# Performance work log

Hardware: AMD Instinct MI355X
Metric: run time of the kernel (lower is better)

Reference implementation:

```python
import jax, jax.numpy as jnp
import numpy as np

D, W, H = 128, 128, 128          # volume obj_shape (d, w, h)
RES_SCALE = 1.4
RES_D = int(D * RES_SCALE)       # 179 detector rows
RES_H = int(H * RES_SCALE)       # 179 detector cols
N_PROJ = 10


def setup_inputs() -> dict:
    key = jax.random.key(0)
    k1, k2 = jax.random.split(key, 2)
    # learnable reconstruction volume, initialized to ones (torch.ones_like)
    I_rec = jnp.ones((1, 1, D, W, H), dtype=jnp.float32)
    # emitter positions, scaled to volume size; y-component kept away from the
    # source plane y=0 so that ray directions are well-conditioned
    poses = jax.random.uniform(k1, (50, 3), dtype=jnp.float32)
    poses = poses * jnp.array([D, W, H], jnp.float32) + jnp.array([-64.0, 256.0, -64.0], jnp.float32)
    idx = jax.random.randint(k2, (N_PROJ,), 0, 50, dtype=jnp.int32)
    return {"I_rec": I_rec, "poses": poses, "idx": idx}


def _trilinear_3d(vol, coords):
    """torch F.grid_sample 3D, bilinear, align_corners=False, zero padding.
    vol: [D, Hd, Wd]; coords: [..., 3] in (x, y, z) normalized to [-1, 1],
    where x indexes the last (Wd) axis, y the middle, z the first."""
    Dv, Hv, Wv = vol.shape
    x, y, z = coords[..., 0], coords[..., 1], coords[..., 2]
    ix = ((x + 1.0) * Wv - 1.0) * 0.5
    iy = ((y + 1.0) * Hv - 1.0) * 0.5
    iz = ((z + 1.0) * Dv - 1.0) * 0.5
    x0f, y0f, z0f = jnp.floor(ix), jnp.floor(iy), jnp.floor(iz)
    tx, ty, tz = ix - x0f, iy - y0f, iz - z0f
    x0 = x0f.astype(jnp.int32); y0 = y0f.astype(jnp.int32); z0 = z0f.astype(jnp.int32)
    x1, y1, z1 = x0 + 1, y0 + 1, z0 + 1

    def gather(zc, yc, xc):
        valid = (zc >= 0) & (zc < Dv) & (yc >= 0) & (yc < Hv) & (xc >= 0) & (xc < Wv)
        v = vol[jnp.clip(zc, 0, Dv - 1), jnp.clip(yc, 0, Hv - 1), jnp.clip(xc, 0, Wv - 1)]
        return jnp.where(valid, v, 0.0)

    out = (
        gather(z0, y0, x0) * (1 - tz) * (1 - ty) * (1 - tx)
        + gather(z0, y0, x1) * (1 - tz) * (1 - ty) * tx
        + gather(z0, y1, x0) * (1 - tz) * ty * (1 - tx)
        + gather(z0, y1, x1) * (1 - tz) * ty * tx
        + gather(z1, y0, x0) * tz * (1 - ty) * (1 - tx)
        + gather(z1, y0, x1) * tz * (1 - ty) * tx
        + gather(z1, y1, x0) * tz * ty * (1 - tx)
        + gather(z1, y1, x1) * tz * ty * tx
    )
    return out


def _project_one(vol, emi):
    """vol: [D, W, H]; emi: [3] emitter position. Returns [RES_D, RES_H]."""
    lin_x = jnp.linspace(-RES_D / 2.0, RES_D / 2.0 - 1.0, RES_D, dtype=jnp.float32)
    lin_y = jnp.linspace(-RES_H / 2.0, RES_H / 2.0 - 1.0, RES_H, dtype=jnp.float32)
    gx, gy = jnp.meshgrid(lin_x, lin_y, indexing="ij")            # [Gx, Gy]
    rays = jnp.stack([gx, jnp.zeros_like(gx), gy], axis=-1) - emi  # [Gx, Gy, 3]
    rays = rays / jnp.linalg.norm(rays, axis=-1, keepdims=True)
    dx = jnp.abs(1.0 / rays[..., 1])                               # [Gx, Gy]
    # (P0 - I0) . N  with N = (0,1,0): source-plane y samples minus emitter y
    p0y = jnp.linspace(0.0, W - 1.0, W, dtype=jnp.float32)         # [K=W]
    T = (1.0 / rays[..., 1])[..., None] * (p0y - emi[1])           # [Gx, Gy, K]
    grid = rays[..., None, :] * T[..., None] + emi                 # [Gx, Gy, K, 3]
    g0 = grid[..., 0] / D * 2.0
    g1 = grid[..., 1] / W * 2.0 - 1.0
    g2 = grid[..., 2] / H * 2.0
    coords = jnp.stack([g2, g1, g0], axis=-1)  # torch.flip(grid, [3]) -> (x,y,z)
    samp = _trilinear_3d(vol, coords)          # [Gx, Gy, K]
    return jnp.sum(samp, axis=-1) * dx


def reference(I_rec, poses, idx):
    sel = poses[idx]  # [10, 3]
    vol = I_rec[0, 0]
    projections = jax.vmap(lambda e: _project_one(vol, e))(sel)  # [10, Gx, Gy]
    return projections[None], idx
```

## Files before the change

### kernel.cpp

```cpp
#include <hip/hip_runtime.h>
#include <hip/hip_bf16.h>
#include <stdint.h>


#define DVOL   128
#define RES    179
#define NPROJ  10
#define OUT_PROJ (NPROJ * RES * RES)
#define BATCH  8

#define IL_A   132
#define IL_C   130
#define IL_SLAB (IL_C * IL_A)
#define IL_TOT  (DVOL * IL_SLAB)

__device__ __forceinline__ float psval(const float* __restrict__ vol, int p, int r, int ai) {
    const int c = r - 1, a = ai - 1;
    if (c < 0 || c >= 128 || a < 0 || a >= 128) return 0.0f;
    const float* src = vol + (c << 14) + (p << 7) + a;
    float v = src[0];
    if (p >= 1) v += src[-128];
    return v;
}

__device__ __forceinline__ uint32_t bfbits(float v) {
    __hip_bfloat16 h = __float2bfloat16(v);
    return (uint32_t)*(unsigned short*)&h;
}

__global__ __launch_bounds__(256) void pad_kernel(const float* __restrict__ vol,
                                                  uint32_t* __restrict__ il) {
    const int t = blockIdx.x * 256 + threadIdx.x;
    if (t >= IL_TOT) return;
    const int p  = t / IL_SLAB;
    const int r  = t - p * IL_SLAB;
    const int ci = r / IL_A;
    const int ai = r - ci * IL_A;
    const float lo = psval(vol, p, ci,     ai);
    const float hi = psval(vol, p, ci + 1, ai);
    il[t] = (bfbits(hi) << 16) | bfbits(lo);
}

__device__ __forceinline__ void axis_interval(float base, float slope, float lo, float hi,
                                              float& t0, float& t1) {
    if (fabsf(slope) < 1e-9f) {
        const bool in = (base >= lo && base <= hi);
        t0 = in ? -1e30f : 1e30f;
        t1 = in ?  1e30f : -1e30f;
    } else {
        const float inv = 1.0f / slope;
        const float a = (lo - base) * inv;
        const float b = (hi - base) * inv;
        t0 = fminf(a, b);
        t1 = fmaxf(a, b);
    }
}

__device__ __forceinline__ int wave_imin(int v) {
    #pragma unroll
    for (int o = 32; o; o >>= 1) v = min(v, __shfl_xor(v, o, 64));
    return v;
}
__device__ __forceinline__ int wave_imax(int v) {
    #pragma unroll
    for (int o = 32; o; o >>= 1) v = max(v, __shfl_xor(v, o, 64));
    return v;
}

__device__ __forceinline__ float asf(uint32_t u) { return __uint_as_float(u); }

__global__ __launch_bounds__(128) void proj_fast(
    const uint32_t* __restrict__ il,
    const float* __restrict__ poses,
    const int* __restrict__ idx,
    float* __restrict__ out)
{
    const int lane = threadIdx.x & 63;
    const int wid  = threadIdx.x >> 6;
    int gj = blockIdx.x * 64 + lane;
    int gi = blockIdx.y * 2 + wid;
    const int j = blockIdx.z;

    if (blockIdx.x == 0 && blockIdx.y == 0 && j == 0 && threadIdx.x < NPROJ)
        out[OUT_PROJ + threadIdx.x] = (float)idx[threadIdx.x];

    const bool store_ok = (gi < RES) && (gj < RES);
    gi = min(gi, RES - 1);
    gj = min(gj, RES - 1);

    const int pid = idx[j];
    const float ex = poses[pid * 3 + 0];
    const float ey = poses[pid * 3 + 1];
    const float ez = poses[pid * 3 + 2];

    const float pdx = (float)gi - 89.5f;
    const float pdz = (float)gj - 89.5f;

    const float inv_ey = 1.0f / ey;
    const float sx = (ex - pdx) * inv_ey;
    const float sz = (ez - pdz) * inv_ey;
    const float ddx = pdx - ex, ddz = pdz - ez;
    const float dxw = sqrtf(ddx * ddx + ey * ey + ddz * ddz) * fabsf(inv_ey);
    const float cb = pdx + 63.5f;
    const float ab = pdz + 63.5f;

    float gc0, gc1, ga0, ga1;
    axis_interval(cb, sx, -1.0f, 128.0f, gc0, gc1);
    axis_interval(ab, sz, -1.0f, 128.0f, ga0, ga1);
    const float q_lo = fmaxf(fmaxf(gc0, ga0), 0.0f);
    const float q_hi = fminf(fminf(gc1, ga1), 127.0f);
    int q0, q1;
    if (q_lo <= q_hi + 0.5f) {
        q0 = max(0, (int)ceilf(q_lo) - 1);
        q1 = min(DVOL, (int)floorf(q_hi) + 2);
    } else { q0 = DVOL; q1 = 0; }
    int Q0 = wave_imin(q0);
    int Q1 = wave_imax(q1);
    Q0 = __builtin_amdgcn_readfirstlane(Q0);
    Q1 = __builtin_amdgcn_readfirstlane(Q1);

    float acc = 0.0f;
    int p = Q0;
    float cf = fmaf((float)Q0, sx, cb);
    float af = fmaf((float)Q0, sz, ab);
    const uint32_t* slab = il + Q0 * IL_SLAB;

    for (; p + (BATCH - 1) < Q1; p += BATCH) {
        float tc[BATCH], ta[BATCH];
        uint2 w[BATCH];
        #pragma unroll
        for (int k = 0; k < BATCH; ++k) {
            const float cfc = fminf(fmaxf(fmaf((float)k, sx, cf), -1.0f), 128.0f);
            const float afc = fminf(fmaxf(fmaf((float)k, sz, af), -1.0f), 128.0f);
            const float c0f = floorf(cfc);
            const float a0f = floorf(afc);
            tc[k] = cfc - c0f;
            ta[k] = afc - a0f;
            const int c0 = __builtin_amdgcn_readfirstlane((int)c0f);
            const int a0 = (int)a0f;
            const uint32_t* wr = slab + k * IL_SLAB + (c0 + 1) * IL_A + 1;
            w[k] = *(const uint2*)(wr + a0);
        }
        #pragma unroll
        for (int k = 0; k < BATCH; ++k) {
            const float f00 = asf(w[k].x << 16);
            const float f10 = asf(w[k].x & 0xffff0000u);
            const float f01 = asf(w[k].y << 16);
            const float f11 = asf(w[k].y & 0xffff0000u);
            const float h0 = fmaf(ta[k], f01 - f00, f00);
            const float h1 = fmaf(ta[k], f11 - f10, f10);
            acc += fmaf(tc[k], h1 - h0, h0);
        }
        cf += (float)BATCH * sx;
        af += (float)BATCH * sz;
        slab += BATCH * IL_SLAB;
    }
    for (; p < Q1; ++p) {
        const float cfc = fminf(fmaxf(cf, -1.0f), 128.0f);
        const float afc = fminf(fmaxf(af, -1.0f), 128.0f);
        const float c0f = floorf(cfc);
        const float a0f = floorf(afc);
        const float tc = cfc - c0f;
        const float ta = afc - a0f;
        const int c0 = __builtin_amdgcn_readfirstlane((int)c0f);
        const int a0 = (int)a0f;
        const uint32_t* wr = slab + (c0 + 1) * IL_A + 1;
        const uint2 w2 = *(const uint2*)(wr + a0);
        const float f00 = asf(w2.x << 16);
        const float f10 = asf(w2.x & 0xffff0000u);
        const float f01 = asf(w2.y << 16);
        const float f11 = asf(w2.y & 0xffff0000u);
        const float h0 = fmaf(ta, f01 - f00, f00);
        const float h1 = fmaf(ta, f11 - f10, f10);
        acc += fmaf(tc, h1 - h0, h0);
        cf += sx; af += sz; slab += IL_SLAB;
    }

    if (store_ok) out[j * (RES * RES) + gi * RES + gj] = acc * (0.5f * dxw);
}

__global__ __launch_bounds__(256) void proj_kernel_fb(
    const float* __restrict__ vol, const float* __restrict__ poses,
    const int* __restrict__ idx, float* __restrict__ out)
{
    const int gj = blockIdx.x * 64 + (threadIdx.x & 63);
    const int gi = blockIdx.y * 4 + (threadIdx.x >> 6);
    const int j  = blockIdx.z;
    if (blockIdx.x == 0 && blockIdx.y == 0 && j == 0 && threadIdx.x < NPROJ)
        out[OUT_PROJ + threadIdx.x] = (float)idx[threadIdx.x];
    if (gi >= RES || gj >= RES) return;
    const int pid = idx[j];
    const float ex = poses[pid*3+0], ey = poses[pid*3+1], ez = poses[pid*3+2];
    const float pdx = (float)gi - 89.5f, pdz = (float)gj - 89.5f;
    const float inv_ey = 1.0f / ey;
    const float sx = (ex - pdx) * inv_ey, sz = (ez - pdz) * inv_ey;
    const float ddx = pdx - ex, ddz = pdz - ez;
    const float dxw = sqrtf(ddx*ddx + ey*ey + ddz*ddz) * fabsf(inv_ey);
    const float cb = pdx + 63.5f, ab = pdz + 63.5f;
    float acc = 0.0f;
    for (int p = 0; p < DVOL; ++p) {
        const float cf = fmaf((float)p, sx, cb);
        const float af = fmaf((float)p, sz, ab);
        if (cf >= -1.0f && cf < 128.0f && af >= -1.0f && af < 128.0f) {
            const float c0f = floorf(cf), a0f = floorf(af);
            const float tc = cf - c0f, ta = af - a0f;
            const int c0 = (int)c0f, a0 = (int)a0f;
            const float wc0 = (c0 >= 0)   ? (1.0f - tc) : 0.0f;
            const float wc1 = (c0 <= 126) ? tc          : 0.0f;
            const float wa0 = (a0 >= 0)   ? (1.0f - ta) : 0.0f;
            const float wa1 = (a0 <= 126) ? ta          : 0.0f;
            const int c0c = c0 < 0 ? 0 : c0;
            const int c1c = c0 >= 127 ? 127 : c0 + 1;
            const int a0c = a0 < 0 ? 0 : a0;
            const int a1c = a0 >= 127 ? 127 : a0 + 1;
            const float w00 = wc0*wa0, w01 = wc0*wa1, w10 = wc1*wa0, w11 = wc1*wa1;
            const int b0 = (c0c << 14) + (p << 7);
            const int b1 = (c1c << 14) + (p << 7);
            float s = w00*vol[b0+a0c] + w01*vol[b0+a1c] + w10*vol[b1+a0c] + w11*vol[b1+a1c];
            if (p >= 1)
                s += w00*vol[b0+a0c-128] + w01*vol[b0+a1c-128]
                   + w10*vol[b1+a0c-128] + w11*vol[b1+a1c-128];
            acc += 0.5f * s;
        }
    }
    out[j * (RES * RES) + gi * RES + gj] = acc * dxw;
}

extern "C" void kernel_launch(void* const* d_in, const int* in_sizes, int n_in,
                              void* d_out, int out_size, void* d_ws, size_t ws_size,
                              hipStream_t stream) {
    const float* vol   = (const float*)d_in[0];
    const float* poses = (const float*)d_in[1];
    const int*   idx   = (const int*)d_in[2];
    float* out = (float*)d_out;

    if (ws_size >= (size_t)IL_TOT * sizeof(uint32_t)) {
        uint32_t* ilbuf = (uint32_t*)d_ws;
        pad_kernel<<<IL_TOT / 256, 256, 0, stream>>>(vol, ilbuf);
        dim3 grid(3 , 90 , NPROJ);
        proj_fast<<<grid, 128, 0, stream>>>(ilbuf, poses, idx, out);
    } else {
        dim3 grid(3, 45, NPROJ);
        proj_kernel_fb<<<grid, 256, 0, stream>>>(vol, poses, idx, out);
    }
}
```

Baseline: 101.4 us.

## Split each ray's depth range across two waves and double-buffer sample loads

Each block now handles one detector row, and its two waves each take half of the ray's depth range. The partial sums are combined through shared memory after a barrier. The batched loop is also restructured to double-buffer: the next 8-sample batch's gathers are issued before the current batch is interpolated, which hides load latency. The grid doubles in the row dimension, and the change adds a __syncthreads, shared memory, and higher register pressure from holding two batches.

```diff
diff --git a/kernel.cpp b/kernel.cpp
--- a/kernel.cpp
+++ b/kernel.cpp
@@ -7,7 +7,6 @@
 #define RES    179
 #define NPROJ  10
 #define OUT_PROJ (NPROJ * RES * RES)
-#define BATCH  8
 
 #define IL_A   132
 #define IL_C   130
@@ -69,23 +68,61 @@
 
 __device__ __forceinline__ float asf(uint32_t u) { return __uint_as_float(u); }
 
+struct B8 { float tc[8], ta[8]; uint2 w[8]; };
+
+__device__ __forceinline__ void load_b8(B8& b, const uint32_t* __restrict__ il, int p,
+                                        float cb, float ab, float sx, float sz) {
+    const uint32_t* slab = il + p * IL_SLAB;
+    const float cf = fmaf((float)p, sx, cb);
+    const float af = fmaf((float)p, sz, ab);
+    #pragma unroll
+    for (int k = 0; k < 8; ++k) {
+        const float cfc = fminf(fmaxf(fmaf((float)k, sx, cf), -1.0f), 128.0f);
+        const float afc = fminf(fmaxf(fmaf((float)k, sz, af), -1.0f), 128.0f);
+        const float c0f = floorf(cfc);
+        const float a0f = floorf(afc);
+        b.tc[k] = cfc - c0f;
+        b.ta[k] = afc - a0f;
+        const int c0 = __builtin_amdgcn_readfirstlane((int)c0f);
+        const int a0 = (int)a0f;
+        const uint32_t* wr = slab + k * IL_SLAB + (c0 + 1) * IL_A + 1;
+        b.w[k] = *(const uint2*)(wr + a0);
+    }
+}
+
+__device__ __forceinline__ float comp_b8(const B8& b) {
+    float s = 0.0f;
+    #pragma unroll
+    for (int k = 0; k < 8; ++k) {
+        const float f00 = asf(b.w[k].x << 16);
+        const float f10 = asf(b.w[k].x & 0xffff0000u);
+        const float f01 = asf(b.w[k].y << 16);
+        const float f11 = asf(b.w[k].y & 0xffff0000u);
+        const float h0 = fmaf(b.ta[k], f01 - f00, f00);
+        const float h1 = fmaf(b.ta[k], f11 - f10, f10);
+        s += fmaf(b.tc[k], h1 - h0, h0);
+    }
+    return s;
+}
+
 __global__ __launch_bounds__(128) void proj_fast(
     const uint32_t* __restrict__ il,
     const float* __restrict__ poses,
     const int* __restrict__ idx,
     float* __restrict__ out)
 {
+    __shared__ float part[64];
+
     const int lane = threadIdx.x & 63;
     const int wid  = threadIdx.x >> 6;
     int gj = blockIdx.x * 64 + lane;
-    int gi = blockIdx.y * 2 + wid;
-    const int j = blockIdx.z;
+    const int gi = blockIdx.y;
+    const int j  = blockIdx.z;
 
     if (blockIdx.x == 0 && blockIdx.y == 0 && j == 0 && threadIdx.x < NPROJ)
         out[OUT_PROJ + threadIdx.x] = (float)idx[threadIdx.x];
 
-    const bool store_ok = (gi < RES) && (gj < RES);
-    gi = min(gi, RES - 1);
+    const bool store_ok = (gj < RES);
     gj = min(gj, RES - 1);
 
     const int pid = idx[j];
@@ -119,52 +156,44 @@
     Q0 = __builtin_amdgcn_readfirstlane(Q0);
     Q1 = __builtin_amdgcn_readfirstlane(Q1);
 
+    const int len = max(0, Q1 - Q0);
+    const int mid = Q0 + (len >> 1);
+    const int r0 = wid ? mid : Q0;
+    const int r1 = wid ? Q1 : mid;
+
     float acc = 0.0f;
-    int p = Q0;
-    float cf = fmaf((float)Q0, sx, cb);
-    float af = fmaf((float)Q0, sz, ab);
-    const uint32_t* slab = il + Q0 * IL_SLAB;
-
-    for (; p + (BATCH - 1) < Q1; p += BATCH) {
-        float tc[BATCH], ta[BATCH];
-        uint2 w[BATCH];
-        #pragma unroll
-        for (int k = 0; k < BATCH; ++k) {
-            const float cfc = fminf(fmaxf(fmaf((float)k, sx, cf), -1.0f), 128.0f);
-            const float afc = fminf(fmaxf(fmaf((float)k, sz, af), -1.0f), 128.0f);
-            const float c0f = floorf(cfc);
-            const float a0f = floorf(afc);
-            tc[k] = cfc - c0f;
-            ta[k] = afc - a0f;
-            const int c0 = __builtin_amdgcn_readfirstlane((int)c0f);
-            const int a0 = (int)a0f;
-            const uint32_t* wr = slab + k * IL_SLAB + (c0 + 1) * IL_A + 1;
-            w[k] = *(const uint2*)(wr + a0);
+    int p = r0;
+    const int nfull = (r1 - r0) >> 3;
+
+    if (nfull > 0) {
+        B8 A, Bb;
+        load_b8(A, il, p, cb, ab, sx, sz);
+        int remaining = nfull;
+        while (remaining >= 2) {
+            load_b8(Bb, il, p + 8, cb, ab, sx, sz);
+            acc += comp_b8(A);
+            p += 8; --remaining;
+            if (remaining >= 2) {
+                load_b8(A, il, p + 8, cb, ab, sx, sz);
+                acc += comp_b8(Bb);
+                p += 8; --remaining;
+            } else {
+                acc += comp_b8(Bb);
+                p += 8; --remaining;
+            }
         }
-        #pragma unroll
-        for (int k = 0; k < BATCH; ++k) {
-            const float f00 = asf(w[k].x << 16);
-            const float f10 = asf(w[k].x & 0xffff0000u);
-            const float f01 = asf(w[k].y << 16);
-            const float f11 = asf(w[k].y & 0xffff0000u);
-            const float h0 = fmaf(ta[k], f01 - f00, f00);
-            const float h1 = fmaf(ta[k], f11 - f10, f10);
-            acc += fmaf(tc[k], h1 - h0, h0);
-        }
-        cf += (float)BATCH * sx;
-        af += (float)BATCH * sz;
-        slab += BATCH * IL_SLAB;
-    }
-    for (; p < Q1; ++p) {
-        const float cfc = fminf(fmaxf(cf, -1.0f), 128.0f);
-        const float afc = fminf(fmaxf(af, -1.0f), 128.0f);
+        if (remaining == 1) { acc += comp_b8(A); p += 8; }
+    }
+    for (; p < r1; ++p) {
+        const float cfc = fminf(fmaxf(fmaf((float)p, sx, cb), -1.0f), 128.0f);
+        const float afc = fminf(fmaxf(fmaf((float)p, sz, ab), -1.0f), 128.0f);
         const float c0f = floorf(cfc);
         const float a0f = floorf(afc);
         const float tc = cfc - c0f;
         const float ta = afc - a0f;
         const int c0 = __builtin_amdgcn_readfirstlane((int)c0f);
         const int a0 = (int)a0f;
-        const uint32_t* wr = slab + (c0 + 1) * IL_A + 1;
+        const uint32_t* wr = il + p * IL_SLAB + (c0 + 1) * IL_A + 1;
         const uint2 w2 = *(const uint2*)(wr + a0);
         const float f00 = asf(w2.x << 16);
         const float f10 = asf(w2.x & 0xffff0000u);
@@ -173,10 +202,12 @@
         const float h0 = fmaf(ta, f01 - f00, f00);
         const float h1 = fmaf(ta, f11 - f10, f10);
         acc += fmaf(tc, h1 - h0, h0);
-        cf += sx; af += sz; slab += IL_SLAB;
-    }
-
-    if (store_ok) out[j * (RES * RES) + gi * RES + gj] = acc * (0.5f * dxw);
+    }
+
+    if (wid == 1) part[lane] = acc;
+    __syncthreads();
+    if (wid == 0 && store_ok)
+        out[j * (RES * RES) + gi * RES + gj] = (acc + part[lane]) * (0.5f * dxw);
 }
 
 __global__ __launch_bounds__(256) void proj_kernel_fb(
@@ -237,7 +268,7 @@
     if (ws_size >= (size_t)IL_TOT * sizeof(uint32_t)) {
         uint32_t* ilbuf = (uint32_t*)d_ws;
         pad_kernel<<<IL_TOT / 256, 256, 0, stream>>>(vol, ilbuf);
-        dim3 grid(3 , 90 , NPROJ);
+        dim3 grid(3 , RES, NPROJ);
         proj_fast<<<grid, 128, 0, stream>>>(ilbuf, poses, idx, out);
     } else {
         dim3 grid(3, 45, NPROJ);
```

Measured after the change: 105.8 us. 4.4% more time.

## Convert projection kernel to persistent wave loop and index pad kernel by 2D grid

Applied to the files above, without the earlier changes.

The projection kernel now launches a fixed grid of 2048 blocks, and each wave strides over (x-tile, row, projection) work items instead of getting one per block. The old grid also launched a padding row when RES is odd, which is now gone. The pad kernel uses a 2D grid over (row, slab), which removes the per-thread integer divisions. Together these aim to cut launch and tail overhead and index arithmetic, at the cost of a modulo/divide per item and possibly worse load balance between waves with different ray lengths.

```diff
diff --git a/kernel.cpp b/kernel.cpp
--- a/kernel.cpp
+++ b/kernel.cpp
@@ -13,6 +13,10 @@
 #define IL_C   130
 #define IL_SLAB (IL_C * IL_A)
 #define IL_TOT  (DVOL * IL_SLAB)
+
+#define ITEMS  (3 * RES * NPROJ)
+#define PBLK   2048
+#define PWAVES (PBLK * 2)
 
 __device__ __forceinline__ float psval(const float* __restrict__ vol, int p, int r, int ai) {
     const int c = r - 1, a = ai - 1;
@@ -28,17 +32,23 @@
     return (uint32_t)*(unsigned short*)&h;
 }
 
-__global__ __launch_bounds__(256) void pad_kernel(const float* __restrict__ vol,
+__global__ __launch_bounds__(128) void pad_kernel(const float* __restrict__ vol,
                                                   uint32_t* __restrict__ il) {
-    const int t = blockIdx.x * 256 + threadIdx.x;
-    if (t >= IL_TOT) return;
-    const int p  = t / IL_SLAB;
-    const int r  = t - p * IL_SLAB;
-    const int ci = r / IL_A;
-    const int ai = r - ci * IL_A;
-    const float lo = psval(vol, p, ci,     ai);
-    const float hi = psval(vol, p, ci + 1, ai);
-    il[t] = (bfbits(hi) << 16) | bfbits(lo);
+    const int ci = blockIdx.x;
+    const int p  = blockIdx.y;
+    const int t  = threadIdx.x;
+    const int base = p * IL_SLAB + ci * IL_A;
+    {
+        const float lo = psval(vol, p, ci,     t);
+        const float hi = psval(vol, p, ci + 1, t);
+        il[base + t] = (bfbits(hi) << 16) | bfbits(lo);
+    }
+    if (t < IL_A - 128) {
+        const int ai = 128 + t;
+        const float lo = psval(vol, p, ci,     ai);
+        const float hi = psval(vol, p, ci + 1, ai);
+        il[base + ai] = (bfbits(hi) << 16) | bfbits(lo);
+    }
 }
 
 __device__ __forceinline__ void axis_interval(float base, float slope, float lo, float hi,
@@ -69,114 +79,118 @@
 
 __device__ __forceinline__ float asf(uint32_t u) { return __uint_as_float(u); }
 
-__global__ __launch_bounds__(128) void proj_fast(
+__global__ __launch_bounds__(128) void proj_persist(
     const uint32_t* __restrict__ il,
     const float* __restrict__ poses,
     const int* __restrict__ idx,
     float* __restrict__ out)
 {
-    const int lane = threadIdx.x & 63;
-    const int wid  = threadIdx.x >> 6;
-    int gj = blockIdx.x * 64 + lane;
-    int gi = blockIdx.y * 2 + wid;
-    const int j = blockIdx.z;
-
-    if (blockIdx.x == 0 && blockIdx.y == 0 && j == 0 && threadIdx.x < NPROJ)
+    const int lane  = threadIdx.x & 63;
+    const int wslot = (blockIdx.x << 1) | (threadIdx.x >> 6);
+
+    if (blockIdx.x == 0 && threadIdx.x < NPROJ)
         out[OUT_PROJ + threadIdx.x] = (float)idx[threadIdx.x];
 
-    const bool store_ok = (gi < RES) && (gj < RES);
-    gi = min(gi, RES - 1);
-    gj = min(gj, RES - 1);
-
-    const int pid = idx[j];
-    const float ex = poses[pid * 3 + 0];
-    const float ey = poses[pid * 3 + 1];
-    const float ez = poses[pid * 3 + 2];
-
-    const float pdx = (float)gi - 89.5f;
-    const float pdz = (float)gj - 89.5f;
-
-    const float inv_ey = 1.0f / ey;
-    const float sx = (ex - pdx) * inv_ey;
-    const float sz = (ez - pdz) * inv_ey;
-    const float ddx = pdx - ex, ddz = pdz - ez;
-    const float dxw = sqrtf(ddx * ddx + ey * ey + ddz * ddz) * fabsf(inv_ey);
-    const float cb = pdx + 63.5f;
-    const float ab = pdz + 63.5f;
-
-    float gc0, gc1, ga0, ga1;
-    axis_interval(cb, sx, -1.0f, 128.0f, gc0, gc1);
-    axis_interval(ab, sz, -1.0f, 128.0f, ga0, ga1);
-    const float q_lo = fmaxf(fmaxf(gc0, ga0), 0.0f);
-    const float q_hi = fminf(fminf(gc1, ga1), 127.0f);
-    int q0, q1;
-    if (q_lo <= q_hi + 0.5f) {
-        q0 = max(0, (int)ceilf(q_lo) - 1);
-        q1 = min(DVOL, (int)floorf(q_hi) + 2);
-    } else { q0 = DVOL; q1 = 0; }
-    int Q0 = wave_imin(q0);
-    int Q1 = wave_imax(q1);
-    Q0 = __builtin_amdgcn_readfirstlane(Q0);
-    Q1 = __builtin_amdgcn_readfirstlane(Q1);
-
-    float acc = 0.0f;
-    int p = Q0;
-    float cf = fmaf((float)Q0, sx, cb);
-    float af = fmaf((float)Q0, sz, ab);
-    const uint32_t* slab = il + Q0 * IL_SLAB;
-
-    for (; p + (BATCH - 1) < Q1; p += BATCH) {
-        float tc[BATCH], ta[BATCH];
-        uint2 w[BATCH];
-        #pragma unroll
-        for (int k = 0; k < BATCH; ++k) {
-            const float cfc = fminf(fmaxf(fmaf((float)k, sx, cf), -1.0f), 128.0f);
-            const float afc = fminf(fmaxf(fmaf((float)k, sz, af), -1.0f), 128.0f);
+    for (int item = wslot; item < ITEMS; item += PWAVES) {
+        const int xtile = item % 3;
+        const int rest  = item / 3;
+        const int gi    = rest % RES;
+        const int j     = rest / RES;
+
+        int gj = xtile * 64 + lane;
+        const bool store_ok = (gj < RES);
+        gj = min(gj, RES - 1);
+
+        const int pid = idx[j];
+        const float ex = poses[pid * 3 + 0];
+        const float ey = poses[pid * 3 + 1];
+        const float ez = poses[pid * 3 + 2];
+
+        const float pdx = (float)gi - 89.5f;
+        const float pdz = (float)gj - 89.5f;
+
+        const float inv_ey = 1.0f / ey;
+        const float sx = (ex - pdx) * inv_ey;
+        const float sz = (ez - pdz) * inv_ey;
+        const float ddx = pdx - ex, ddz = pdz - ez;
+        const float dxw = sqrtf(ddx * ddx + ey * ey + ddz * ddz) * fabsf(inv_ey);
+        const float cb = pdx + 63.5f;
+        const float ab = pdz + 63.5f;
+
+        float gc0, gc1, ga0, ga1;
+        axis_interval(cb, sx, -1.0f, 128.0f, gc0, gc1);
+        axis_interval(ab, sz, -1.0f, 128.0f, ga0, ga1);
+        const float q_lo = fmaxf(fmaxf(gc0, ga0), 0.0f);
+        const float q_hi = fminf(fminf(gc1, ga1), 127.0f);
+        int q0, q1;
+        if (q_lo <= q_hi + 0.5f) {
+            q0 = max(0, (int)ceilf(q_lo) - 1);
+            q1 = min(DVOL, (int)floorf(q_hi) + 2);
+        } else { q0 = DVOL; q1 = 0; }
+        int Q0 = wave_imin(q0);
+        int Q1 = wave_imax(q1);
+        Q0 = __builtin_amdgcn_readfirstlane(Q0);
+        Q1 = __builtin_amdgcn_readfirstlane(Q1);
+
+        float acc = 0.0f;
+        int p = Q0;
+        float cf = fmaf((float)Q0, sx, cb);
+        float af = fmaf((float)Q0, sz, ab);
+        const uint32_t* slab = il + Q0 * IL_SLAB;
+
+        for (; p + (BATCH - 1) < Q1; p += BATCH) {
+            float tc[BATCH], ta[BATCH];
+            uint2 w[BATCH];
+            #pragma unroll
+            for (int k = 0; k < BATCH; ++k) {
+                const float cfc = fminf(fmaxf(fmaf((float)k, sx, cf), -1.0f), 128.0f);
+                const float afc = fminf(fmaxf(fmaf((float)k, sz, af), -1.0f), 128.0f);
+                const float c0f = floorf(cfc);
+                const float a0f = floorf(afc);
+                tc[k] = cfc - c0f;
+                ta[k] = afc - a0f;
+                const int c0 = __builtin_amdgcn_readfirstlane((int)c0f);
+                const int a0 = (int)a0f;
+                const uint32_t* wr = slab + k * IL_SLAB + (c0 + 1) * IL_A + 1;
+                w[k] = *(const uint2*)(wr + a0);
+            }
+            #pragma unroll
+            for (int k = 0; k < BATCH; ++k) {
+                const float f00 = asf(w[k].x << 16);
+                const float f10 = asf(w[k].x & 0xffff0000u);
+                const float f01 = asf(w[k].y << 16);
+                const float f11 = asf(w[k].y & 0xffff0000u);
+                const float h0 = fmaf(ta[k], f01 - f00, f00);
+                const float h1 = fmaf(ta[k], f11 - f10, f10);
+                acc += fmaf(tc[k], h1 - h0, h0);
+            }
+            cf += (float)BATCH * sx;
+            af += (float)BATCH * sz;
+            slab += BATCH * IL_SLAB;
+        }
+        for (; p < Q1; ++p) {
+            const float cfc = fminf(fmaxf(cf, -1.0f), 128.0f);
+            const float afc = fminf(fmaxf(af, -1.0f), 128.0f);
             const float c0f = floorf(cfc);
             const float a0f = floorf(afc);
-            tc[k] = cfc - c0f;
-            ta[k] = afc - a0f;
+            const float tc = cfc - c0f;
+            const float ta = afc - a0f;
             const int c0 = __builtin_amdgcn_readfirstlane((int)c0f);
             const int a0 = (int)a0f;
-            const uint32_t* wr = slab + k * IL_SLAB + (c0 + 1) * IL_A + 1;
-            w[k] = *(const uint2*)(wr + a0);
+            const uint32_t* wr = slab + (c0 + 1) * IL_A + 1;
+            const uint2 w2 = *(const uint2*)(wr + a0);
+            const float f00 = asf(w2.x << 16);
+            const float f10 = asf(w2.x & 0xffff0000u);
+            const float f01 = asf(w2.y << 16);
+            const float f11 = asf(w2.y & 0xffff0000u);
+            const float h0 = fmaf(ta, f01 - f00, f00);
+            const float h1 = fmaf(ta, f11 - f10, f10);
+            acc += fmaf(tc, h1 - h0, h0);
+            cf += sx; af += sz; slab += IL_SLAB;
         }
-        #pragma unroll
-        for (int k = 0; k < BATCH; ++k) {
-            const float f00 = asf(w[k].x << 16);
-            const float f10 = asf(w[k].x & 0xffff0000u);
-            const float f01 = asf(w[k].y << 16);
-            const float f11 = asf(w[k].y & 0xffff0000u);
-            const float h0 = fmaf(ta[k], f01 - f00, f00);
-            const float h1 = fmaf(ta[k], f11 - f10, f10);
-            acc += fmaf(tc[k], h1 - h0, h0);
-        }
-        cf += (float)BATCH * sx;
-        af += (float)BATCH * sz;
-        slab += BATCH * IL_SLAB;
-    }
-    for (; p < Q1; ++p) {
-        const float cfc = fminf(fmaxf(cf, -1.0f), 128.0f);
-        const float afc = fminf(fmaxf(af, -1.0f), 128.0f);
-        const float c0f = floorf(cfc);
-        const float a0f = floorf(afc);
-        const float tc = cfc - c0f;
-        const float ta = afc - a0f;
-        const int c0 = __builtin_amdgcn_readfirstlane((int)c0f);
-        const int a0 = (int)a0f;
-        const uint32_t* wr = slab + (c0 + 1) * IL_A + 1;
-        const uint2 w2 = *(const uint2*)(wr + a0);
-        const float f00 = asf(w2.x << 16);
-        const float f10 = asf(w2.x & 0xffff0000u);
-        const float f01 = asf(w2.y << 16);
-        const float f11 = asf(w2.y & 0xffff0000u);
-        const float h0 = fmaf(ta, f01 - f00, f00);
-        const float h1 = fmaf(ta, f11 - f10, f10);
-        acc += fmaf(tc, h1 - h0, h0);
-        cf += sx; af += sz; slab += IL_SLAB;
-    }
-
-    if (store_ok) out[j * (RES * RES) + gi * RES + gj] = acc * (0.5f * dxw);
+
+        if (store_ok) out[j * (RES * RES) + gi * RES + gj] = acc * (0.5f * dxw);
+    }
 }
 
 __global__ __launch_bounds__(256) void proj_kernel_fb(
@@ -236,9 +250,9 @@
 
     if (ws_size >= (size_t)IL_TOT * sizeof(uint32_t)) {
         uint32_t* ilbuf = (uint32_t*)d_ws;
-        pad_kernel<<<IL_TOT / 256, 256, 0, stream>>>(vol, ilbuf);
-        dim3 grid(3 , 90 , NPROJ);
-        proj_fast<<<grid, 128, 0, stream>>>(ilbuf, poses, idx, out);
+        dim3 pgrid(IL_C, DVOL);
+        pad_kernel<<<pgrid, 128, 0, stream>>>(vol, ilbuf);
+        proj_persist<<<PBLK, 128, 0, stream>>>(ilbuf, poses, idx, out);
     } else {
         dim3 grid(3, 45, NPROJ);
         proj_kernel_fb<<<grid, 256, 0, stream>>>(vol, poses, idx, out);
```

Result: slower. 106.9 us (+5.4%).

## Restructure pad kernel to reuse column values and precompute per-wave slab offsets in LDS

Applied to the files above, without the earlier changes.

The pad kernel now gives each thread a column strip and walks down rows, carrying the previous row's bf16 value so each volume element is loaded once instead of twice, and it zeroes the border entries explicitly. The projection kernel precomputes, per wave, the per-slab row fraction and base offset into a shared-memory table, so the main loop reads them instead of recomputing the floor/clamp and readfirstlane each step. This trims ALU work in the hot loop and halves global reads in padding, at the cost of an LDS table, an extra prologue pass, and dropping the scalar readfirstlane hint for the row index.

```diff
diff --git a/kernel.cpp b/kernel.cpp
--- a/kernel.cpp
+++ b/kernel.cpp
@@ -14,31 +14,48 @@
 #define IL_SLAB (IL_C * IL_A)
 #define IL_TOT  (DVOL * IL_SLAB)
 
-__device__ __forceinline__ float psval(const float* __restrict__ vol, int p, int r, int ai) {
-    const int c = r - 1, a = ai - 1;
-    if (c < 0 || c >= 128 || a < 0 || a >= 128) return 0.0f;
-    const float* src = vol + (c << 14) + (p << 7) + a;
-    float v = src[0];
-    if (p >= 1) v += src[-128];
-    return v;
-}
-
 __device__ __forceinline__ uint32_t bfbits(float v) {
     __hip_bfloat16 h = __float2bfloat16(v);
     return (uint32_t)*(unsigned short*)&h;
 }
 
-__global__ __launch_bounds__(256) void pad_kernel(const float* __restrict__ vol,
+__global__ __launch_bounds__(128) void pad_kernel(const float* __restrict__ vol,
                                                   uint32_t* __restrict__ il) {
-    const int t = blockIdx.x * 256 + threadIdx.x;
-    if (t >= IL_TOT) return;
-    const int p  = t / IL_SLAB;
-    const int r  = t - p * IL_SLAB;
-    const int ci = r / IL_A;
-    const int ai = r - ci * IL_A;
-    const float lo = psval(vol, p, ci,     ai);
-    const float hi = psval(vol, p, ci + 1, ai);
-    il[t] = (bfbits(hi) << 16) | bfbits(lo);
+    const int q = blockIdx.x;
+    const int p = blockIdx.y;
+    const int a = threadIdx.x;
+    const int wlo = q * 17;
+    const int whi = min(130, wlo + 17);
+    uint32_t* slab = il + p * IL_SLAB;
+
+    uint32_t prev = 0;
+    {
+        const int c = wlo - 1;
+        if (c >= 0 && c < 128) {
+            const float* src = vol + (c << 14) + (p << 7) + a;
+            float v = src[0];
+            if (p >= 1) v += src[-128];
+            prev = bfbits(v);
+        }
+    }
+    #pragma unroll 2
+    for (int c = wlo; c < whi; ++c) {
+        uint32_t cur = 0;
+        if (c < 128) {
+            const float* src = vol + (c << 14) + (p << 7) + a;
+            float v = src[0];
+            if (p >= 1) v += src[-128];
+            cur = bfbits(v);
+        }
+        slab[c * IL_A + (a + 1)] = (cur << 16) | prev;
+        prev = cur;
+    }
+    for (int b = a; b < (whi - wlo) * 4; b += 128) {
+        const int w  = wlo + (b >> 2);
+        const int bi = b & 3;
+        const int ai = (bi == 0) ? 0 : (128 + bi);
+        slab[w * IL_A + ai] = 0u;
+    }
 }
 
 __device__ __forceinline__ void axis_interval(float base, float slope, float lo, float hi,
@@ -75,6 +92,8 @@
     const int* __restrict__ idx,
     float* __restrict__ out)
 {
+    __shared__ uint2 tab[2][DVOL];
+
     const int lane = threadIdx.x & 63;
     const int wid  = threadIdx.x >> 6;
     int gj = blockIdx.x * 64 + lane;
@@ -119,27 +138,34 @@
     Q0 = __builtin_amdgcn_readfirstlane(Q0);
     Q1 = __builtin_amdgcn_readfirstlane(Q1);
 
+    const int n = Q1 - Q0;
+    for (int e = lane; e < n; e += 64) {
+        const int p = Q0 + e;
+        const float cfc = fminf(fmaxf(fmaf((float)p, sx, cb), -1.0f), 128.0f);
+        const float c0f = floorf(cfc);
+        const int c0 = (int)c0f;
+        uint2 t;
+        t.x = __float_as_uint(cfc - c0f);
+        t.y = (uint32_t)(p * IL_SLAB + (c0 + 1) * IL_A + 1);
+        tab[wid][e] = t;
+    }
+
     float acc = 0.0f;
-    int p = Q0;
-    float cf = fmaf((float)Q0, sx, cb);
+    int pe = 0;
     float af = fmaf((float)Q0, sz, ab);
-    const uint32_t* slab = il + Q0 * IL_SLAB;
-
-    for (; p + (BATCH - 1) < Q1; p += BATCH) {
+
+    for (; pe + (BATCH - 1) < n; pe += BATCH) {
         float tc[BATCH], ta[BATCH];
         uint2 w[BATCH];
         #pragma unroll
         for (int k = 0; k < BATCH; ++k) {
-            const float cfc = fminf(fmaxf(fmaf((float)k, sx, cf), -1.0f), 128.0f);
+            const uint2 t = tab[wid][pe + k];
+            tc[k] = asf(t.x);
             const float afc = fminf(fmaxf(fmaf((float)k, sz, af), -1.0f), 128.0f);
-            const float c0f = floorf(cfc);
             const float a0f = floorf(afc);
-            tc[k] = cfc - c0f;
             ta[k] = afc - a0f;
-            const int c0 = __builtin_amdgcn_readfirstlane((int)c0f);
             const int a0 = (int)a0f;
-            const uint32_t* wr = slab + k * IL_SLAB + (c0 + 1) * IL_A + 1;
-            w[k] = *(const uint2*)(wr + a0);
+            w[k] = *(const uint2*)(il + t.y + a0);
         }
         #pragma unroll
         for (int k = 0; k < BATCH; ++k) {
@@ -151,21 +177,16 @@
             const float h1 = fmaf(ta[k], f11 - f10, f10);
             acc += fmaf(tc[k], h1 - h0, h0);
         }
-        cf += (float)BATCH * sx;
         af += (float)BATCH * sz;
-        slab += BATCH * IL_SLAB;
-    }
-    for (; p < Q1; ++p) {
-        const float cfc = fminf(fmaxf(cf, -1.0f), 128.0f);
+    }
+    for (; pe < n; ++pe) {
+        const uint2 t = tab[wid][pe];
+        const float tc = asf(t.x);
         const float afc = fminf(fmaxf(af, -1.0f), 128.0f);
-        const float c0f = floorf(cfc);
         const float a0f = floorf(afc);
-        const float tc = cfc - c0f;
         const float ta = afc - a0f;
-        const int c0 = __builtin_amdgcn_readfirstlane((int)c0f);
         const int a0 = (int)a0f;
-        const uint32_t* wr = slab + (c0 + 1) * IL_A + 1;
-        const uint2 w2 = *(const uint2*)(wr + a0);
+        const uint2 w2 = *(const uint2*)(il + t.y + a0);
         const float f00 = asf(w2.x << 16);
         const float f10 = asf(w2.x & 0xffff0000u);
         const float f01 = asf(w2.y << 16);
@@ -173,7 +194,7 @@
         const float h0 = fmaf(ta, f01 - f00, f00);
         const float h1 = fmaf(ta, f11 - f10, f10);
         acc += fmaf(tc, h1 - h0, h0);
-        cf += sx; af += sz; slab += IL_SLAB;
+        af += sz;
     }
 
     if (store_ok) out[j * (RES * RES) + gi * RES + gj] = acc * (0.5f * dxw);
@@ -236,7 +257,8 @@
 
     if (ws_size >= (size_t)IL_TOT * sizeof(uint32_t)) {
         uint32_t* ilbuf = (uint32_t*)d_ws;
-        pad_kernel<<<IL_TOT / 256, 256, 0, stream>>>(vol, ilbuf);
+        dim3 pgrid(8, DVOL);
+        pad_kernel<<<pgrid, 128, 0, stream>>>(vol, ilbuf);
         dim3 grid(3 , 90 , NPROJ);
         proj_fast<<<grid, 128, 0, stream>>>(ilbuf, poses, idx, out);
     } else {
```

Measured after the change: 93.63 us (median of 2 runs). 1.08x faster.
